# Optimization experiments

Hardware: AMD Instinct MI355X
Metric: run time of the kernel (lower is better)

## Reference

```python
import jax, jax.numpy as jnp
import numpy as np

B, N, CHANNELS = 4, 2048, 512
HEADS, HEAD_DIM = 8, 64
HIDDEN = HEADS * HEAD_DIM
ROPE_THETA = 10000.0


def _rotate_half(x):
    # interleaved pairs, as in rotary_embedding_torch
    x1 = x[..., 0::2]
    x2 = x[..., 1::2]
    return jnp.stack((-x2, x1), axis=-1).reshape(x.shape)


def _rope(x):
    # x: [b, h, n, d]; rotate over seq axis -2, full head dim
    n, d = x.shape[-2], x.shape[-1]
    inv_freq = 1.0 / (ROPE_THETA ** (jnp.arange(0, d, 2, dtype=jnp.float32) / d))
    freqs = jnp.arange(n, dtype=jnp.float32)[:, None] * inv_freq  # [n, d/2]
    freqs = jnp.repeat(freqs, 2, axis=-1)  # [n, d]
    return x * jnp.cos(freqs) + _rotate_half(x) * jnp.sin(freqs)


def setup_inputs() -> dict:
    key = jax.random.key(0)
    k1, k2, k3, k4 = jax.random.split(key, 4)
    x = jax.random.normal(k1, (B, N, CHANNELS), dtype=jnp.float32)
    pos_bias = jax.random.normal(k2, (HEADS, N, N), dtype=jnp.float32) * 0.02
    w_qkv = jax.random.normal(k3, (3 * HIDDEN, CHANNELS), dtype=jnp.float32) / np.sqrt(CHANNELS)
    w_out = jax.random.normal(k4, (CHANNELS, HIDDEN), dtype=jnp.float32) / np.sqrt(HIDDEN)
    return {"x": x, "pos_bias": pos_bias, "w_qkv": w_qkv, "w_out": w_out}


def reference(x, pos_bias, w_qkv, w_out):
    scale = HEAD_DIM ** -0.5
    b, n, _ = x.shape
    qkv = x @ w_qkv.T  # [b, n, 3*hidden]
    q, k, v = jnp.split(qkv, 3, axis=-1)

    def split_heads(z):
        return z.reshape(b, n, HEADS, HEAD_DIM).transpose(0, 2, 1, 3)  # [b,h,n,d]

    q, k, v = map(split_heads, (q, k, v))
    q = q * scale
    q = _rope(q)
    k = _rope(k)
    sim = jnp.einsum('bhid,bhjd->bhij', q, k) + pos_bias  # pos_bias [h,n,n] broadcasts
    attn = jax.nn.softmax(sim, axis=-1)  # matches sim - amax(detached) then softmax
    out = jnp.einsum('bhij,bhjd->bhid', attn, v)
    out = out.transpose(0, 2, 1, 3).reshape(b, n, HIDDEN)
    return out @ w_out.T
```

## Files before the change

kernel.cpp:

```cpp
#include <hip/hip_runtime.h>
#include <hip/hip_bf16.h>
#include <math.h>

typedef __bf16 bf16;
typedef bf16  bf16x8 __attribute__((ext_vector_type(8)));
typedef bf16  bf16x4 __attribute__((ext_vector_type(4)));
typedef float f32x4  __attribute__((ext_vector_type(4)));
typedef float f32x16 __attribute__((ext_vector_type(16)));

#define B_   4
#define N_   2048
#define CH_  512
#define H_   8
#define D_   64
#define HID_ 512

__device__ __forceinline__ f32x4 mfma16(bf16x8 a, bf16x8 b, f32x4 c) {
    return __builtin_amdgcn_mfma_f32_16x16x32_bf16(a, b, c, 0, 0, 0);
}
__device__ __forceinline__ f32x16 mfma32(bf16x8 a, bf16x8 b, f32x16 c) {
    return __builtin_amdgcn_mfma_f32_32x32x16_bf16(a, b, c, 0, 0, 0);
}

#define GLL(src, dst) __builtin_amdgcn_global_load_lds( \
        (const __attribute__((address_space(1))) unsigned int*)(src), \
        (__attribute__((address_space(3))) unsigned int*)(dst), 16, 0, 0)

__global__ __launch_bounds__(256) void prep_k(
    const float* __restrict__ x, const float* __restrict__ wq, const float* __restrict__ wo,
    bf16* __restrict__ xb, bf16* __restrict__ wqb, bf16* __restrict__ wob)
{
    const int NX = 4194304 / 4, NQ = 786432 / 4, NO = 262144 / 4;
    const int total = NX + NQ + NO;
    for (int idx = blockIdx.x * 256 + threadIdx.x; idx < total; idx += gridDim.x * 256) {
        const float4* src; bf16* dst; int off;
        if (idx < NX)           { src = (const float4*)x;  dst = xb;  off = idx; }
        else if (idx < NX + NQ) { src = (const float4*)wq; dst = wqb; off = idx - NX; }
        else                    { src = (const float4*)wo; dst = wob; off = idx - NX - NQ; }
        float4 v = src[off];
        bf16x4 o = { (bf16)v.x, (bf16)v.y, (bf16)v.z, (bf16)v.w };
        *reinterpret_cast<bf16x4*>(dst + (size_t)off * 4) = o;
    }
}

__global__ void rope_table_k(float* __restrict__ cosT, float* __restrict__ sinT) {
    int idx = blockIdx.x * 256 + threadIdx.x;
    int pos = idx >> 5, fi = idx & 31;
    double inv = pow(10000.0, -(double)(2 * fi) / 64.0);
    double ang = (double)pos * inv;
    cosT[idx] = (float)cos(ang);
    sinT[idx] = (float)sin(ang);
}

__global__ __launch_bounds__(256) void qkv_rope_k(
    const bf16* __restrict__ xb, const bf16* __restrict__ wb,
    const float* __restrict__ cosT, const float* __restrict__ sinT,
    bf16* __restrict__ Qb, bf16* __restrict__ Kb, bf16* __restrict__ Vt)
{
    __shared__ __align__(16) unsigned char Xs[2][16384];
    __shared__ __align__(16) unsigned char Ws[2][16384];
    const int tid = threadIdx.x, lane = tid & 63, wid = tid >> 6;
    const int wr = wid >> 1, wc = wid & 1;
    const int m0 = blockIdx.x * 128, n0 = blockIdx.y * 128;
    const int l15 = lane & 15, l4 = lane >> 4;

    const unsigned scol = ((lane & 7) * 16) ^ ((lane >> 3) << 4);
    const char* ag = (const char*)xb + (size_t)(m0 + wid * 32 + (lane >> 3)) * 1024 + scol;
    const char* bg = (const char*)wb + (size_t)(n0 + wid * 32 + (lane >> 3)) * 1024 + scol;

#define QSTAGE(buf, kt) do { \
        _Pragma("unroll") \
        for (int g = 0; g < 4; ++g) { \
            GLL(ag + (size_t)(kt) * 128 + (size_t)g * 8192, &Xs[buf][wid * 4096 + g * 1024]); \
            GLL(bg + (size_t)(kt) * 128 + (size_t)g * 8192, &Ws[buf][wid * 4096 + g * 1024]); \
        } \
    } while (0)

    f32x4 acc[4][4] = {};

    QSTAGE(0, 0);
    __syncthreads();

    for (int kt = 0; kt < 8; ++kt) {
        const int cur = kt & 1;
        if (kt < 7) QSTAGE(cur ^ 1, kt + 1);
#pragma unroll
        for (int ks = 0; ks < 2; ++ks) {
            bf16x8 a[4], bb[4];
#pragma unroll
            for (int mf = 0; mf < 4; ++mf) {
                const int row = wr * 64 + mf * 16 + l15;
                a[mf] = *reinterpret_cast<const bf16x8*>(
                    &Xs[cur][row * 128 + ((ks * 64 + l4 * 16) ^ ((l15 & 7) << 4))]);
            }
#pragma unroll
            for (int nf = 0; nf < 4; ++nf) {
                const int row = wc * 64 + nf * 16 + l15;
                bb[nf] = *reinterpret_cast<const bf16x8*>(
                    &Ws[cur][row * 128 + ((ks * 64 + l4 * 16) ^ ((l15 & 7) << 4))]);
            }
#pragma unroll
            for (int mf = 0; mf < 4; ++mf)
#pragma unroll
                for (int nf = 0; nf < 4; ++nf)
                    acc[mf][nf] = mfma16(a[mf], bb[nf], acc[mf][nf]);
        }
        __syncthreads();
    }

#pragma unroll
    for (int nf = 0; nf < 4; ++nf) {
        const int col = n0 + wc * 64 + nf * 16 + l15;
        const int sec = col >> 9;
        const int cc = col & 511;
        const int hh = cc >> 6, dd = cc & 63;
        if (sec == 2) {
#pragma unroll
            for (int mf = 0; mf < 4; ++mf) {
                const int pos0 = m0 + wr * 64 + mf * 16 + l4 * 4;
                const int bb_ = pos0 >> 11, pos = pos0 & 2047;
                bf16x4 pk = { (bf16)acc[mf][nf][0], (bf16)acc[mf][nf][1],
                              (bf16)acc[mf][nf][2], (bf16)acc[mf][nf][3] };
                *reinterpret_cast<bf16x4*>(
                    Vt + ((size_t)(bb_ * H_ + hh) * D_ + dd) * N_ + pos) = pk;
            }
        } else {
            const float sgn = (dd & 1) ? 1.f : -1.f;
#pragma unroll
            for (int mf = 0; mf < 4; ++mf) {
#pragma unroll
                for (int i = 0; i < 4; ++i) {
                    const int row = m0 + wr * 64 + mf * 16 + l4 * 4 + i;
                    const int bb_ = row >> 11, pos = row & 2047;
                    const float v = acc[mf][nf][i];
                    const float v2 = __shfl_xor(v, 1);
                    const size_t dst = ((size_t)((bb_ * H_ + hh) * N_ + pos)) * D_ + dd;
                    const float c = cosT[pos * 32 + (dd >> 1)];
                    const float s = sinT[pos * 32 + (dd >> 1)];
                    const float r = v * c + sgn * v2 * s;
                    if (sec == 0) Qb[dst] = (bf16)(r * 0.125f);
                    else          Kb[dst] = (bf16)r;
                }
            }
        }
    }
}

#define KRD2(kt2,kc) (((kt2)*32 + l31)*128 + (((kc)*32 + l5*16) ^ (l7<<4)))
#define VRD2(dt,kt)  (((dt)*32 + l31)*128 + (((kt)*32 + l5*16) ^ (l7<<4)))
#define PRD2(kt)     (wid*4096 + l31*128 + (((kt)*32 + l5*16) ^ (l7<<4)))
#define PST2(kt2,r2) (wid*4096 + l31*128 + (((kt2)*64 + (r2)*16 + l5*8) ^ (l7<<4)))

__global__ __launch_bounds__(128, 2) void attn_k(
    const bf16* __restrict__ Qb, const bf16* __restrict__ Kb, const bf16* __restrict__ Vt,
    const float* __restrict__ bias, bf16* __restrict__ AO)
{
    __shared__ __align__(16) unsigned char KsB[2][8192];
    __shared__ __align__(16) unsigned char VsB[2][8192];
    __shared__ __align__(16) unsigned char PwB[2][4096];

    const int tid = threadIdx.x, lane = tid & 63, wid = tid >> 6;
    const int l31 = lane & 31, l5 = lane >> 5, l7 = lane & 7;
    const int id = blockIdx.x;
    const int xcd = id & 7, j = id >> 3;
    const int bh = xcd + 8 * (j >> 5);
    const int qt = j & 31;
    const int b = bh >> 3, h = bh & 7;
    const int q0 = qt * 64 + wid * 32;
    const size_t bhoff = (size_t)bh * N_ * D_;

    bf16x8 qreg[4];
#pragma unroll
    for (int kc = 0; kc < 4; ++kc)
        qreg[kc] = *reinterpret_cast<const bf16x8*>(
            Qb + bhoff + (size_t)(q0 + l31) * D_ + kc * 16 + l5 * 8);

    const unsigned scol = ((lane & 7) * 16) ^ ((lane >> 3) << 4);
    const char* kg = (const char*)(Kb + bhoff) + (size_t)(wid * 32 + (lane >> 3)) * 128 + scol;
    const char* vg = (const char*)(Vt + bhoff) + (size_t)(wid * 32 + (lane >> 3)) * (N_ * 2) + scol;

    const float* bp = bias + ((size_t)h * N_ + (q0 + l31)) * N_ + l5 * 4;

    unsigned char* pwD = &PwB[0][0];

#define STAGE(buf, t) do { \
        GLL(kg + (size_t)(t) * 8192,            &KsB[buf][wid * 4096]); \
        GLL(kg + (size_t)(t) * 8192 + 1024,     &KsB[buf][wid * 4096 + 1024]); \
        GLL(kg + (size_t)(t) * 8192 + 2048,     &KsB[buf][wid * 4096 + 2048]); \
        GLL(kg + (size_t)(t) * 8192 + 3072,     &KsB[buf][wid * 4096 + 3072]); \
        GLL(vg + (size_t)(t) * 128,             &VsB[buf][wid * 4096]); \
        GLL(vg + (size_t)(t) * 128 + 32768,     &VsB[buf][wid * 4096 + 1024]); \
        GLL(vg + (size_t)(t) * 128 + 65536,     &VsB[buf][wid * 4096 + 2048]); \
        GLL(vg + (size_t)(t) * 128 + 98304,     &VsB[buf][wid * 4096 + 3072]); \
    } while (0)

    f32x16 o[2] = {};
    float lp = 0.f;
    f32x4 bc[2][4], bn[2][4];

    STAGE(0, 0);
#pragma unroll
    for (int kt2 = 0; kt2 < 2; ++kt2)
#pragma unroll
        for (int r2 = 0; r2 < 4; ++r2)
            bc[kt2][r2] = *reinterpret_cast<const f32x4*>(bp + kt2 * 32 + r2 * 8);
    __syncthreads();

#pragma unroll 2
    for (int kb = 0; kb < 32; ++kb) {
        const int cur = kb & 1;
        if (kb < 31) {
            STAGE(cur ^ 1, kb + 1);
#pragma unroll
            for (int kt2 = 0; kt2 < 2; ++kt2)
#pragma unroll
                for (int r2 = 0; r2 < 4; ++r2)
                    bn[kt2][r2] = *reinterpret_cast<const f32x4*>(
                        bp + (size_t)(kb + 1) * 64 + kt2 * 32 + r2 * 8);
        }

        const unsigned char* ksC = &KsB[cur][0];
        f32x16 s[2] = {};
        __builtin_amdgcn_s_setprio(1);
#pragma unroll
        for (int kt2 = 0; kt2 < 2; ++kt2) {
#pragma unroll
            for (int kc = 0; kc < 4; ++kc) {
                bf16x8 kf = *reinterpret_cast<const bf16x8*>(ksC + KRD2(kt2, kc));
                s[kt2] = mfma32(kf, qreg[kc], s[kt2]);
            }
        }
        __builtin_amdgcn_s_setprio(0);

#pragma unroll
        for (int kt2 = 0; kt2 < 2; ++kt2) {
#pragma unroll
            for (int r2 = 0; r2 < 4; ++r2) {
                float p0 = __expf(s[kt2][r2 * 4 + 0] + bc[kt2][r2][0]);
                float p1 = __expf(s[kt2][r2 * 4 + 1] + bc[kt2][r2][1]);
                float p2 = __expf(s[kt2][r2 * 4 + 2] + bc[kt2][r2][2]);
                float p3 = __expf(s[kt2][r2 * 4 + 3] + bc[kt2][r2][3]);
                lp += (p0 + p1) + (p2 + p3);
                bf16x4 pk = { (bf16)p0, (bf16)p1, (bf16)p2, (bf16)p3 };
                *reinterpret_cast<bf16x4*>(pwD + PST2(kt2, r2)) = pk;
            }
        }

        const unsigned char* vsC = &VsB[cur][0];
        __builtin_amdgcn_s_setprio(1);
#pragma unroll
        for (int kt = 0; kt < 4; ++kt) {
            bf16x8 pa = *reinterpret_cast<const bf16x8*>(pwD + PRD2(kt));
#pragma unroll
            for (int dt = 0; dt < 2; ++dt) {
                bf16x8 vf = *reinterpret_cast<const bf16x8*>(vsC + VRD2(dt, kt));
                o[dt] = mfma32(pa, vf, o[dt]);
            }
        }
        __builtin_amdgcn_s_setprio(0);

#pragma unroll
        for (int kt2 = 0; kt2 < 2; ++kt2)
#pragma unroll
            for (int r2 = 0; r2 < 4; ++r2)
                bc[kt2][r2] = bn[kt2][r2];
        __syncthreads();
    }

    float tot = lp;
    tot += __shfl_xor(tot, 32);
    float rv[16];
#pragma unroll
    for (int reg = 0; reg < 16; ++reg) {
        const int qr = (reg & 3) + 8 * (reg >> 2) + 4 * l5;
        rv[reg] = 1.0f / __shfl(tot, qr);
    }
#pragma unroll
    for (int dt = 0; dt < 2; ++dt)
#pragma unroll
        for (int reg = 0; reg < 16; ++reg) {
            const int qr = (reg & 3) + 8 * (reg >> 2) + 4 * l5;
            AO[((size_t)(b * N_ + q0 + qr)) * HID_ + h * D_ + dt * 32 + l31] =
                (bf16)(o[dt][reg] * rv[reg]);
        }
}

__global__ __launch_bounds__(256) void proj_k(
    const bf16* __restrict__ A, const bf16* __restrict__ wob, float* __restrict__ out)
{
    __shared__ __align__(16) unsigned char Xs[2][16384];
    __shared__ __align__(16) unsigned char Ws[2][16384];
    const int tid = threadIdx.x, lane = tid & 63, wid = tid >> 6;
    const int wr = wid >> 1, wc = wid & 1;
    const int m0 = blockIdx.x * 128, n0 = blockIdx.y * 128;
    const int l15 = lane & 15, l4 = lane >> 4;

    const unsigned scol = ((lane & 7) * 16) ^ ((lane >> 3) << 4);
    const char* ag = (const char*)A   + (size_t)(m0 + wid * 32 + (lane >> 3)) * 1024 + scol;
    const char* bg = (const char*)wob + (size_t)(n0 + wid * 32 + (lane >> 3)) * 1024 + scol;

#define PSTAGE(buf, kt) do { \
        _Pragma("unroll") \
        for (int g = 0; g < 4; ++g) { \
            GLL(ag + (size_t)(kt) * 128 + (size_t)g * 8192, &Xs[buf][wid * 4096 + g * 1024]); \
            GLL(bg + (size_t)(kt) * 128 + (size_t)g * 8192, &Ws[buf][wid * 4096 + g * 1024]); \
        } \
    } while (0)

    f32x4 acc[4][4] = {};

    PSTAGE(0, 0);
    __syncthreads();

    for (int kt = 0; kt < 8; ++kt) {
        const int cur = kt & 1;
        if (kt < 7) PSTAGE(cur ^ 1, kt + 1);
#pragma unroll
        for (int ks = 0; ks < 2; ++ks) {
            bf16x8 a[4], bb[4];
#pragma unroll
            for (int mf = 0; mf < 4; ++mf) {
                const int row = wr * 64 + mf * 16 + l15;
                a[mf] = *reinterpret_cast<const bf16x8*>(
                    &Xs[cur][row * 128 + ((ks * 64 + l4 * 16) ^ ((l15 & 7) << 4))]);
            }
#pragma unroll
            for (int nf = 0; nf < 4; ++nf) {
                const int row = wc * 64 + nf * 16 + l15;
                bb[nf] = *reinterpret_cast<const bf16x8*>(
                    &Ws[cur][row * 128 + ((ks * 64 + l4 * 16) ^ ((l15 & 7) << 4))]);
            }
#pragma unroll
            for (int mf = 0; mf < 4; ++mf)
#pragma unroll
                for (int nf = 0; nf < 4; ++nf)
                    acc[mf][nf] = mfma16(a[mf], bb[nf], acc[mf][nf]);
        }
        __syncthreads();
    }

#pragma unroll
    for (int nf = 0; nf < 4; ++nf) {
        const int col = n0 + wc * 64 + nf * 16 + l15;
#pragma unroll
        for (int mf = 0; mf < 4; ++mf) {
#pragma unroll
            for (int i = 0; i < 4; ++i) {
                const int row = m0 + wr * 64 + mf * 16 + l4 * 4 + i;
                out[(size_t)row * HID_ + col] = acc[mf][nf][i];
            }
        }
    }
}

extern "C" void kernel_launch(void* const* d_in, const int* in_sizes, int n_in,
                              void* d_out, int out_size, void* d_ws, size_t ws_size,
                              hipStream_t stream) {
    (void)in_sizes; (void)n_in; (void)out_size; (void)ws_size;
    const float* x     = (const float*)d_in[0];
    const float* bias  = (const float*)d_in[1];
    const float* w_qkv = (const float*)d_in[2];
    const float* w_out = (const float*)d_in[3];
    float* out = (float*)d_out;

    bf16* base = (bf16*)d_ws;
    bf16* Qb = base;
    bf16* Kb = base + 4194304;
    bf16* Vt = base + 8388608;
    bf16* AO = base + 12582912;
    bf16* xb = AO;
    float* cosT = (float*)(base + 16777216);
    float* sinT = cosT + 65536;
    bf16* wqb = (bf16*)(sinT + 65536);
    bf16* wob = wqb + 786432;

    prep_k      <<<dim3(2560), 256, 0, stream>>>(x, w_qkv, w_out, xb, wqb, wob);
    rope_table_k<<<dim3(256), 256, 0, stream>>>(cosT, sinT);
    qkv_rope_k  <<<dim3(64, 12), 256, 0, stream>>>(xb, wqb, cosT, sinT, Qb, Kb, Vt);
    attn_k      <<<dim3(1024), 128, 0, stream>>>(Qb, Kb, Vt, bias, AO);
    proj_k      <<<dim3(64, 4), 256, 0, stream>>>(AO, wob, out);
}
```

Baseline: 131.0 us.

## Split attention over key halves, keep P in registers, deepen bias prefetch

The attention kernel now splits the key range into two halves per query tile, doubling the grid to 2048 blocks. It writes unnormalized partial outputs and row sums, and a new merge kernel combines them. The P tile now moves from the score layout to the MFMA A-operand layout with cross-half-wave shuffles instead of an LDS round trip. Bias loads are prefetched two iterations ahead, and the plain __syncthreads is replaced with a partial vmcnt wait plus barrier. This is meant to improve occupancy and latency hiding, at the cost of an extra kernel launch, extra global traffic for partials, and a precision loss from storing unnormalized partial sums in bf16.

```diff
diff --git a/kernel.cpp b/kernel.cpp
--- a/kernel.cpp
+++ b/kernel.cpp
@@ -7,6 +7,8 @@
 typedef bf16  bf16x4 __attribute__((ext_vector_type(4)));
 typedef float f32x4  __attribute__((ext_vector_type(4)));
 typedef float f32x16 __attribute__((ext_vector_type(16)));
+typedef unsigned int u32x2 __attribute__((ext_vector_type(2)));
+typedef unsigned int u32x4 __attribute__((ext_vector_type(4)));
 
 #define B_   4
 #define N_   2048
@@ -148,25 +150,25 @@
 
 #define KRD2(kt2,kc) (((kt2)*32 + l31)*128 + (((kc)*32 + l5*16) ^ (l7<<4)))
 #define VRD2(dt,kt)  (((dt)*32 + l31)*128 + (((kt)*32 + l5*16) ^ (l7<<4)))
-#define PRD2(kt)     (wid*4096 + l31*128 + (((kt)*32 + l5*16) ^ (l7<<4)))
-#define PST2(kt2,r2) (wid*4096 + l31*128 + (((kt2)*64 + (r2)*16 + l5*8) ^ (l7<<4)))
 
 __global__ __launch_bounds__(128, 2) void attn_k(
     const bf16* __restrict__ Qb, const bf16* __restrict__ Kb, const bf16* __restrict__ Vt,
-    const float* __restrict__ bias, bf16* __restrict__ AO)
+    const float* __restrict__ bias, bf16* __restrict__ AO,
+    bf16* __restrict__ Op1, float* __restrict__ Lp)
 {
     __shared__ __align__(16) unsigned char KsB[2][8192];
     __shared__ __align__(16) unsigned char VsB[2][8192];
-    __shared__ __align__(16) unsigned char PwB[2][4096];
 
     const int tid = threadIdx.x, lane = tid & 63, wid = tid >> 6;
     const int l31 = lane & 31, l5 = lane >> 5, l7 = lane & 7;
     const int id = blockIdx.x;
     const int xcd = id & 7, j = id >> 3;
-    const int bh = xcd + 8 * (j >> 5);
-    const int qt = j & 31;
+    const int bh = xcd + 8 * (j >> 6);
+    const int j2 = j & 63;
+    const int qt = j2 >> 1, kh = j2 & 1;
     const int b = bh >> 3, h = bh & 7;
     const int q0 = qt * 64 + wid * 32;
+    const int k0 = kh * 1024;
     const size_t bhoff = (size_t)bh * N_ * D_;
 
     bf16x8 qreg[4];
@@ -176,12 +178,10 @@
             Qb + bhoff + (size_t)(q0 + l31) * D_ + kc * 16 + l5 * 8);
 
     const unsigned scol = ((lane & 7) * 16) ^ ((lane >> 3) << 4);
-    const char* kg = (const char*)(Kb + bhoff) + (size_t)(wid * 32 + (lane >> 3)) * 128 + scol;
-    const char* vg = (const char*)(Vt + bhoff) + (size_t)(wid * 32 + (lane >> 3)) * (N_ * 2) + scol;
-
-    const float* bp = bias + ((size_t)h * N_ + (q0 + l31)) * N_ + l5 * 4;
-
-    unsigned char* pwD = &PwB[0][0];
+    const char* kg = (const char*)(Kb + bhoff) + (size_t)(k0 + wid * 32 + (lane >> 3)) * 128 + scol;
+    const char* vg = (const char*)(Vt + bhoff) + (size_t)(wid * 32 + (lane >> 3)) * (N_ * 2) + k0 * 2 + scol;
+
+    const float* bp = bias + ((size_t)h * N_ + (q0 + l31)) * N_ + k0 + l5 * 4;
 
 #define STAGE(buf, t) do { \
         GLL(kg + (size_t)(t) * 8192,            &KsB[buf][wid * 4096]); \
@@ -194,29 +194,42 @@
         GLL(vg + (size_t)(t) * 128 + 98304,     &VsB[buf][wid * 4096 + 3072]); \
     } while (0)
 
+#define PIPE_SYNC() do { \
+        asm volatile("s_waitcnt vmcnt(8)" ::: "memory"); \
+        __builtin_amdgcn_sched_barrier(0); \
+        __builtin_amdgcn_s_barrier(); \
+        __builtin_amdgcn_sched_barrier(0); \
+    } while (0)
+
     f32x16 o[2] = {};
     float lp = 0.f;
-    f32x4 bc[2][4], bn[2][4];
+    f32x4 bc[2][4], bn[2][4], b2[2][4];
 
     STAGE(0, 0);
+    __builtin_amdgcn_sched_barrier(0);
 #pragma unroll
     for (int kt2 = 0; kt2 < 2; ++kt2)
 #pragma unroll
-        for (int r2 = 0; r2 < 4; ++r2)
+        for (int r2 = 0; r2 < 4; ++r2) {
             bc[kt2][r2] = *reinterpret_cast<const f32x4*>(bp + kt2 * 32 + r2 * 8);
-    __syncthreads();
+            bn[kt2][r2] = *reinterpret_cast<const f32x4*>(bp + 64 + kt2 * 32 + r2 * 8);
+        }
+    PIPE_SYNC();
 
 #pragma unroll 2
-    for (int kb = 0; kb < 32; ++kb) {
+    for (int kb = 0; kb < 16; ++kb) {
         const int cur = kb & 1;
-        if (kb < 31) {
+        if (kb < 15) {
             STAGE(cur ^ 1, kb + 1);
+            __builtin_amdgcn_sched_barrier(0);
+        }
+        if (kb < 14) {
 #pragma unroll
             for (int kt2 = 0; kt2 < 2; ++kt2)
 #pragma unroll
                 for (int r2 = 0; r2 < 4; ++r2)
-                    bn[kt2][r2] = *reinterpret_cast<const f32x4*>(
-                        bp + (size_t)(kb + 1) * 64 + kt2 * 32 + r2 * 8);
+                    b2[kt2][r2] = *reinterpret_cast<const f32x4*>(
+                        bp + (size_t)(kb + 2) * 64 + kt2 * 32 + r2 * 8);
         }
 
         const unsigned char* ksC = &KsB[cur][0];
@@ -232,8 +245,10 @@
         }
         __builtin_amdgcn_s_setprio(0);
 
+        bf16x8 pa[4];
 #pragma unroll
         for (int kt2 = 0; kt2 < 2; ++kt2) {
+            unsigned U[4][2], R[4][2];
 #pragma unroll
             for (int r2 = 0; r2 < 4; ++r2) {
                 float p0 = __expf(s[kt2][r2 * 4 + 0] + bc[kt2][r2][0]);
@@ -242,7 +257,24 @@
                 float p3 = __expf(s[kt2][r2 * 4 + 3] + bc[kt2][r2][3]);
                 lp += (p0 + p1) + (p2 + p3);
                 bf16x4 pk = { (bf16)p0, (bf16)p1, (bf16)p2, (bf16)p3 };
-                *reinterpret_cast<bf16x4*>(pwD + PST2(kt2, r2)) = pk;
+                u32x2 uu = __builtin_bit_cast(u32x2, pk);
+                U[r2][0] = uu[0];
+                U[r2][1] = uu[1];
+            }
+#pragma unroll
+            for (int r2 = 0; r2 < 4; ++r2) {
+                R[r2][0] = __shfl_xor(U[r2][0], 32);
+                R[r2][1] = __shfl_xor(U[r2][1], 32);
+            }
+            const bool hi = (l5 != 0);
+#pragma unroll
+            for (int ktp = 0; ktp < 2; ++ktp) {
+                unsigned g0 = hi ? R[2 * ktp + 1][0] : U[2 * ktp][0];
+                unsigned g1 = hi ? R[2 * ktp + 1][1] : U[2 * ktp][1];
+                unsigned h0 = hi ? U[2 * ktp + 1][0] : R[2 * ktp][0];
+                unsigned h1 = hi ? U[2 * ktp + 1][1] : R[2 * ktp][1];
+                u32x4 wv = { g0, g1, h0, h1 };
+                pa[kt2 * 2 + ktp] = __builtin_bit_cast(bf16x8, wv);
             }
         }
 
@@ -250,11 +282,10 @@
         __builtin_amdgcn_s_setprio(1);
 #pragma unroll
         for (int kt = 0; kt < 4; ++kt) {
-            bf16x8 pa = *reinterpret_cast<const bf16x8*>(pwD + PRD2(kt));
 #pragma unroll
             for (int dt = 0; dt < 2; ++dt) {
                 bf16x8 vf = *reinterpret_cast<const bf16x8*>(vsC + VRD2(dt, kt));
-                o[dt] = mfma32(pa, vf, o[dt]);
+                o[dt] = mfma32(pa[kt], vf, o[dt]);
             }
         }
         __builtin_amdgcn_s_setprio(0);
@@ -262,27 +293,65 @@
 #pragma unroll
         for (int kt2 = 0; kt2 < 2; ++kt2)
 #pragma unroll
-            for (int r2 = 0; r2 < 4; ++r2)
+            for (int r2 = 0; r2 < 4; ++r2) {
                 bc[kt2][r2] = bn[kt2][r2];
-        __syncthreads();
+                bn[kt2][r2] = b2[kt2][r2];
+            }
+
+        PIPE_SYNC();
     }
 
     float tot = lp;
     tot += __shfl_xor(tot, 32);
-    float rv[16];
-#pragma unroll
-    for (int reg = 0; reg < 16; ++reg) {
-        const int qr = (reg & 3) + 8 * (reg >> 2) + 4 * l5;
-        rv[reg] = 1.0f / __shfl(tot, qr);
-    }
-#pragma unroll
-    for (int dt = 0; dt < 2; ++dt)
-#pragma unroll
-        for (int reg = 0; reg < 16; ++reg) {
-            const int qr = (reg & 3) + 8 * (reg >> 2) + 4 * l5;
-            AO[((size_t)(b * N_ + q0 + qr)) * HID_ + h * D_ + dt * 32 + l31] =
-                (bf16)(o[dt][reg] * rv[reg]);
-        }
+    const int slot = (bh * 32 + qt) * 2 + kh;
+    if (l5 == 0) Lp[slot * 64 + wid * 32 + l31] = tot;
+
+    if (kh == 0) {
+#pragma unroll
+        for (int dt = 0; dt < 2; ++dt)
+#pragma unroll
+            for (int reg = 0; reg < 16; ++reg) {
+                const int qr = (reg & 3) + 8 * (reg >> 2) + 4 * l5;
+                AO[((size_t)(b * N_ + q0 + qr)) * HID_ + h * D_ + dt * 32 + l31] =
+                    (bf16)o[dt][reg];
+            }
+    } else {
+        bf16* op = Op1 + ((size_t)(bh * 32 + qt) * 64) * 64;
+#pragma unroll
+        for (int dt = 0; dt < 2; ++dt)
+#pragma unroll
+            for (int reg = 0; reg < 16; ++reg) {
+                const int qr = (reg & 3) + 8 * (reg >> 2) + 4 * l5;
+                op[(wid * 32 + qr) * 64 + dt * 32 + l31] = (bf16)o[dt][reg];
+            }
+    }
+}
+
+__global__ __launch_bounds__(256) void merge_k(
+    bf16* __restrict__ AO, const bf16* __restrict__ Op1, const float* __restrict__ Lp)
+{
+    const int sp = blockIdx.x;
+    const int bh = sp >> 5, qt = sp & 31;
+    const int b = bh >> 3, h = bh & 7;
+    const int tid = threadIdx.x;
+    const int qq = tid >> 2, d0 = (tid & 3) * 16;
+
+    const float denom = Lp[(sp * 2 + 0) * 64 + qq] + Lp[(sp * 2 + 1) * 64 + qq];
+    const float rinv = 1.0f / denom;
+
+    bf16* aop = AO + ((size_t)(b * N_ + qt * 64 + qq)) * HID_ + h * D_ + d0;
+    const bf16* o1p = Op1 + ((size_t)sp * 64 + qq) * 64 + d0;
+
+#pragma unroll
+    for (int g = 0; g < 2; ++g) {
+        bf16x8 a = *reinterpret_cast<const bf16x8*>(aop + g * 8);
+        bf16x8 c = *reinterpret_cast<const bf16x8*>(o1p + g * 8);
+        bf16x8 r;
+#pragma unroll
+        for (int e = 0; e < 8; ++e)
+            r[e] = (bf16)(((float)a[e] + (float)c[e]) * rinv);
+        *reinterpret_cast<bf16x8*>(aop + g * 8) = r;
+    }
 }
 
 __global__ __launch_bounds__(256) void proj_k(
@@ -373,10 +442,13 @@
     float* sinT = cosT + 65536;
     bf16* wqb = (bf16*)(sinT + 65536);
     bf16* wob = wqb + 786432;
+    bf16* Op1 = wob + 262144;
+    float* Lp = (float*)(Op1 + 4194304);
 
     prep_k      <<<dim3(2560), 256, 0, stream>>>(x, w_qkv, w_out, xb, wqb, wob);
     rope_table_k<<<dim3(256), 256, 0, stream>>>(cosT, sinT);
     qkv_rope_k  <<<dim3(64, 12), 256, 0, stream>>>(xb, wqb, cosT, sinT, Qb, Kb, Vt);
-    attn_k      <<<dim3(1024), 128, 0, stream>>>(Qb, Kb, Vt, bias, AO);
+    attn_k      <<<dim3(2048), 128, 0, stream>>>(Qb, Kb, Vt, bias, AO, Op1, Lp);
+    merge_k     <<<dim3(1024), 256, 0, stream>>>(AO, Op1, Lp);
     proj_k      <<<dim3(64, 4), 256, 0, stream>>>(AO, wob, out);
 }
```

New measurement: 157.1 us. +19.9%, slower.

## Software-pipeline QK^T one tile ahead of softmax and PV

Applied to the files above, without the earlier changes.

Splits K and V staging so that K tiles are prefetched two iterations ahead and V tiles one ahead. Each iteration computes the QK^T scores for the next key block while it runs exp/softmax and the PV MFMAs on the current block's precomputed scores. A prologue computes the first score tile. The aim is to let MFMA work overlap the exp and bf16-pack ALU work and hide LDS latency, at the cost of an extra 32 accumulator registers, which may reduce occupancy.

```diff
diff --git a/kernel.cpp b/kernel.cpp
--- a/kernel.cpp
+++ b/kernel.cpp
@@ -183,11 +183,14 @@
 
     unsigned char* pwD = &PwB[0][0];
 
-#define STAGE(buf, t) do { \
+#define STAGE_K(buf, t) do { \
         GLL(kg + (size_t)(t) * 8192,            &KsB[buf][wid * 4096]); \
         GLL(kg + (size_t)(t) * 8192 + 1024,     &KsB[buf][wid * 4096 + 1024]); \
         GLL(kg + (size_t)(t) * 8192 + 2048,     &KsB[buf][wid * 4096 + 2048]); \
         GLL(kg + (size_t)(t) * 8192 + 3072,     &KsB[buf][wid * 4096 + 3072]); \
+    } while (0)
+
+#define STAGE_V(buf, t) do { \
         GLL(vg + (size_t)(t) * 128,             &VsB[buf][wid * 4096]); \
         GLL(vg + (size_t)(t) * 128 + 32768,     &VsB[buf][wid * 4096 + 1024]); \
         GLL(vg + (size_t)(t) * 128 + 65536,     &VsB[buf][wid * 4096 + 2048]); \
@@ -195,10 +198,13 @@
     } while (0)
 
     f32x16 o[2] = {};
+    f32x16 sA[2] = {};
     float lp = 0.f;
     f32x4 bc[2][4], bn[2][4];
 
-    STAGE(0, 0);
+    STAGE_K(0, 0);
+    STAGE_K(1, 1);
+    STAGE_V(0, 0);
 #pragma unroll
     for (int kt2 = 0; kt2 < 2; ++kt2)
 #pragma unroll
@@ -206,11 +212,26 @@
             bc[kt2][r2] = *reinterpret_cast<const f32x4*>(bp + kt2 * 32 + r2 * 8);
     __syncthreads();
 
+    {
+        const unsigned char* ksC = &KsB[0][0];
+        __builtin_amdgcn_s_setprio(1);
+#pragma unroll
+        for (int kt2 = 0; kt2 < 2; ++kt2)
+#pragma unroll
+            for (int kc = 0; kc < 4; ++kc) {
+                bf16x8 kf = *reinterpret_cast<const bf16x8*>(ksC + KRD2(kt2, kc));
+                sA[kt2] = mfma32(kf, qreg[kc], sA[kt2]);
+            }
+        __builtin_amdgcn_s_setprio(0);
+    }
+    __syncthreads();
+
 #pragma unroll 2
     for (int kb = 0; kb < 32; ++kb) {
         const int cur = kb & 1;
+        if (kb < 30) STAGE_K(cur, kb + 2);
         if (kb < 31) {
-            STAGE(cur ^ 1, kb + 1);
+            STAGE_V(cur ^ 1, kb + 1);
 #pragma unroll
             for (int kt2 = 0; kt2 < 2; ++kt2)
 #pragma unroll
@@ -219,27 +240,26 @@
                         bp + (size_t)(kb + 1) * 64 + kt2 * 32 + r2 * 8);
         }
 
-        const unsigned char* ksC = &KsB[cur][0];
-        f32x16 s[2] = {};
-        __builtin_amdgcn_s_setprio(1);
+        f32x16 sB[2] = {};
+        if (kb < 31) {
+            const unsigned char* ksC = &KsB[cur ^ 1][0];
+#pragma unroll
+            for (int kt2 = 0; kt2 < 2; ++kt2)
+#pragma unroll
+                for (int kc = 0; kc < 4; ++kc) {
+                    bf16x8 kf = *reinterpret_cast<const bf16x8*>(ksC + KRD2(kt2, kc));
+                    sB[kt2] = mfma32(kf, qreg[kc], sB[kt2]);
+                }
+        }
+
 #pragma unroll
         for (int kt2 = 0; kt2 < 2; ++kt2) {
 #pragma unroll
-            for (int kc = 0; kc < 4; ++kc) {
-                bf16x8 kf = *reinterpret_cast<const bf16x8*>(ksC + KRD2(kt2, kc));
-                s[kt2] = mfma32(kf, qreg[kc], s[kt2]);
-            }
-        }
-        __builtin_amdgcn_s_setprio(0);
-
-#pragma unroll
-        for (int kt2 = 0; kt2 < 2; ++kt2) {
-#pragma unroll
             for (int r2 = 0; r2 < 4; ++r2) {
-                float p0 = __expf(s[kt2][r2 * 4 + 0] + bc[kt2][r2][0]);
-                float p1 = __expf(s[kt2][r2 * 4 + 1] + bc[kt2][r2][1]);
-                float p2 = __expf(s[kt2][r2 * 4 + 2] + bc[kt2][r2][2]);
-                float p3 = __expf(s[kt2][r2 * 4 + 3] + bc[kt2][r2][3]);
+                float p0 = __expf(sA[kt2][r2 * 4 + 0] + bc[kt2][r2][0]);
+                float p1 = __expf(sA[kt2][r2 * 4 + 1] + bc[kt2][r2][1]);
+                float p2 = __expf(sA[kt2][r2 * 4 + 2] + bc[kt2][r2][2]);
+                float p3 = __expf(sA[kt2][r2 * 4 + 3] + bc[kt2][r2][3]);
                 lp += (p0 + p1) + (p2 + p3);
                 bf16x4 pk = { (bf16)p0, (bf16)p1, (bf16)p2, (bf16)p3 };
                 *reinterpret_cast<bf16x4*>(pwD + PST2(kt2, r2)) = pk;
@@ -259,6 +279,8 @@
         }
         __builtin_amdgcn_s_setprio(0);
 
+        sA[0] = sB[0];
+        sA[1] = sB[1];
 #pragma unroll
         for (int kt2 = 0; kt2 < 2; ++kt2)
 #pragma unroll
```

New measurement: 145.7 us. 11.2% more time.
